# Optimization experiments

Measured on AMD Instinct MI355X. Metric: run time of the kernel, lower is better.

The kernel has to match this reference:

```python
import jax, jax.numpy as jnp
import numpy as np

N_NODES = 100000
N_EDGES = 1250000
NFEAT = 64
NHID = 64


def setup_inputs() -> dict:
    key = jax.random.key(0)
    k1, k2, k3 = jax.random.split(key, 3)
    x = jax.random.normal(k1, (N_NODES, NFEAT), dtype=jnp.float32)
    edge_index = jax.random.randint(k2, (2, N_EDGES), 0, N_NODES, dtype=jnp.int64)
    # Glorot-style init for the GCNConv weight [out, in]
    scale = 1.0 / np.sqrt(NFEAT)
    weight = jax.random.normal(k3, (NHID, NFEAT), dtype=jnp.float32) * scale
    bias = jnp.zeros((NHID,), dtype=jnp.float32)
    return {"x": x, "edge_index": edge_index, "weight": weight, "bias": bias}


def reference(x, edge_index, weight, bias):
    """Single-layer GCNConv: out = D^-1/2 (A+I) D^-1/2 (x W^T) + b."""
    n = x.shape[0]
    # add self-loops
    loop = jnp.arange(n, dtype=edge_index.dtype)
    src = jnp.concatenate([edge_index[0], loop])  # [E+N]
    dst = jnp.concatenate([edge_index[1], loop])
    # linear transform first (cheaper: nfeat -> nhid)
    h = x @ weight.T  # [N, nhid]
    # symmetric normalization with unit edge weights
    ones = jnp.ones_like(dst, dtype=h.dtype)
    deg = jax.ops.segment_sum(ones, dst, num_segments=n)  # [N]
    dinv = jnp.where(deg > 0, jax.lax.rsqrt(jnp.maximum(deg, 1e-12)), 0.0)
    norm = dinv[src] * dinv[dst]  # [E+N]
    # gather -> scale -> scatter-add
    msg = h[src] * norm[:, None]  # [E+N, nhid]
    out = jax.ops.segment_sum(msg, dst, num_segments=n)  # [N, nhid]
    return out + bias
```

## Files before the change

### kernel.cpp

```cpp
#include <hip/hip_runtime.h>

#define NF 64
#define ELLS 48
#define OCAP 65536


__global__ __launch_bounds__(256) void k_ell(const int* __restrict__ src,
                                             const int* __restrict__ dst,
                                             int* degc, int* ocnt, int* oflow,
                                             int* __restrict__ ell, int e, int n) {
    int grp = blockIdx.x & 7;
    int chunk = (n + 7) >> 3;
    int lo = grp * chunk;
    int hi = min(lo + chunk, n);
    int nb = gridDim.x >> 3;
    int bi = blockIdx.x >> 3;
    for (int i = bi * 256 + threadIdx.x; i < e; i += nb * 256) {
        int d = dst[i];
        if (d < lo || d >= hi) continue;
        int s = src[i];
        int slot = atomicAdd(&degc[d], 1);
        if (slot < ELLS) {
            ell[(long)d * ELLS + slot] = s;
        } else {
            int o = atomicAdd(ocnt, 1);
            if (o < OCAP) { oflow[2 * o] = s; oflow[2 * o + 1] = d; }
        }
    }
}

__global__ __launch_bounds__(256) void k_dinv(const int* __restrict__ degc,
                                              float* __restrict__ dinv, int n) {
    int i = blockIdx.x * 256 + threadIdx.x;
    if (i < n) dinv[i] = rsqrtf((float)(degc[i] + 1));
}


__global__ __launch_bounds__(256) void k_agg_gemm(const float* __restrict__ x,
                                                  const float* __restrict__ W,
                                                  const float* __restrict__ bias,
                                                  const float* __restrict__ dinv,
                                                  const int* __restrict__ degc,
                                                  const int* __restrict__ ell,
                                                  float* __restrict__ out, int n) {
    __shared__ float wt[NF * NF];
    __shared__ float vsh[4][NF];
    int tid = threadIdx.x;
    for (int idx = tid; idx < NF * NF; idx += 256) {
        int k = idx >> 6, j = idx & 63;
        wt[idx] = W[j * NF + k];
    }
    int wv = tid >> 6, lane = tid & 63;
    float bj = bias[lane];
    __syncthreads();

    int ngroups = (n + 3) >> 2, gs = gridDim.x;
    int g = blockIdx.x;
    int d = g * 4 + wv;
    int ev = 0, mc = 0;
    if (d < n) {
        if (lane < ELLS) ev = ell[(long)d * ELLS + lane];
        mc = degc[d];
    }
    while (g < ngroups) {
        int gn = g + gs, dn = gn * 4 + wv;
        int evn = 0, mcn = 0;
        if (gn < ngroups && dn < n) {
            if (lane < ELLS) evn = ell[(long)dn * ELLS + lane];
            mcn = degc[dn];
        }
        if (d < n) {
            float dd = rsqrtf((float)(mc + 1));
            int m = min(mc, ELLS);
            float a0 = x[(long)d * NF + lane] * dd;
            float a1 = 0.f, a2 = 0.f, a3 = 0.f, a4 = 0.f, a5 = 0.f, a6 = 0.f, a7 = 0.f;
            for (int j = 0; j < m; j += 8) {
                int s0 = __shfl(ev, j + 0), s1 = __shfl(ev, j + 1);
                int s2 = __shfl(ev, j + 2), s3 = __shfl(ev, j + 3);
                int s4 = __shfl(ev, j + 4), s5 = __shfl(ev, j + 5);
                int s6 = __shfl(ev, j + 6), s7 = __shfl(ev, j + 7);
                bool b0 = j + 0 < m, b1 = j + 1 < m, b2 = j + 2 < m, b3 = j + 3 < m;
                bool b4 = j + 4 < m, b5 = j + 5 < m, b6 = j + 6 < m, b7 = j + 7 < m;
                s0 = b0 ? s0 : 0; s1 = b1 ? s1 : 0; s2 = b2 ? s2 : 0; s3 = b3 ? s3 : 0;
                s4 = b4 ? s4 : 0; s5 = b5 ? s5 : 0; s6 = b6 ? s6 : 0; s7 = b7 ? s7 : 0;
                float w0 = b0 ? dinv[s0] : 0.f, w1 = b1 ? dinv[s1] : 0.f;
                float w2 = b2 ? dinv[s2] : 0.f, w3 = b3 ? dinv[s3] : 0.f;
                float w4 = b4 ? dinv[s4] : 0.f, w5 = b5 ? dinv[s5] : 0.f;
                float w6 = b6 ? dinv[s6] : 0.f, w7 = b7 ? dinv[s7] : 0.f;
                a0 = fmaf(x[(long)s0 * NF + lane], w0, a0);
                a1 = fmaf(x[(long)s1 * NF + lane], w1, a1);
                a2 = fmaf(x[(long)s2 * NF + lane], w2, a2);
                a3 = fmaf(x[(long)s3 * NF + lane], w3, a3);
                a4 = fmaf(x[(long)s4 * NF + lane], w4, a4);
                a5 = fmaf(x[(long)s5 * NF + lane], w5, a5);
                a6 = fmaf(x[(long)s6 * NF + lane], w6, a6);
                a7 = fmaf(x[(long)s7 * NF + lane], w7, a7);
            }
            float v = dd * (((a0 + a1) + (a2 + a3)) + ((a4 + a5) + (a6 + a7)));

            vsh[wv][lane] = v;
            float r = bj;
#pragma unroll
            for (int k0 = 0; k0 < NF; k0 += 4) {
                float4 bv = *reinterpret_cast<const float4*>(&vsh[wv][k0]);
                r = fmaf(bv.x, wt[(k0 + 0) * NF + lane], r);
                r = fmaf(bv.y, wt[(k0 + 1) * NF + lane], r);
                r = fmaf(bv.z, wt[(k0 + 2) * NF + lane], r);
                r = fmaf(bv.w, wt[(k0 + 3) * NF + lane], r);
            }
            out[(long)d * NF + lane] = r;
        }
        g = gn; d = dn; ev = evn; mc = mcn;
    }
}

__global__ __launch_bounds__(64) void k_oflow(const float* __restrict__ x,
                                              const float* __restrict__ W,
                                              const float* __restrict__ dinv,
                                              const int* __restrict__ ocnt,
                                              const int* __restrict__ oflow,
                                              float* out) {
    int c = *ocnt; if (c > OCAP) c = OCAP;
    int lane = threadIdx.x;
    for (int o = blockIdx.x; o < c; o += gridDim.x) {
        int s = oflow[2 * o], d = oflow[2 * o + 1];
        float norm = dinv[s] * dinv[d];
        float r = 0.f;
        for (int k = 0; k < NF; ++k)
            r = fmaf(x[(long)s * NF + k], W[lane * NF + k], r);
        atomicAdd(&out[(long)d * NF + lane], norm * r);
    }
}


extern "C" void kernel_launch(void* const* d_in, const int* in_sizes, int n_in,
                              void* d_out, int out_size, void* d_ws, size_t ws_size,
                              hipStream_t stream) {
    const float* x    = (const float*)d_in[0];
    const int*   ei   = (const int*)d_in[1];
    const float* W    = (const float*)d_in[2];
    const float* bias = (const float*)d_in[3];
    float*       out  = (float*)d_out;

    const int n = in_sizes[0] / NF;
    const int e = in_sizes[1] / 2;
    const int* src = ei;
    const int* dst = ei + e;

    int*   degc  = (int*)d_ws;
    int*   ocnt  = degc + n;
    float* dinv  = (float*)(ocnt + 1);
    int*   oflow = (int*)(dinv + n);
    int*   ell   = oflow + 2 * OCAP;

    dim3 blk(256);
    hipMemsetAsync(degc, 0, (size_t)(n + 1) * sizeof(int), stream);
    k_ell <<<2048, blk, 0, stream>>>(src, dst, degc, ocnt, oflow, ell, e, n);
    k_dinv<<<(n + 255) / 256, blk, 0, stream>>>(degc, dinv, n);
    k_agg_gemm<<<2048, blk, 0, stream>>>(x, W, bias, dinv, degc, ell, out, n);
    k_oflow<<<64, 64, 0, stream>>>(x, W, dinv, ocnt, oflow, out);
}
```

Before: 146.4 us.

## Gather fp16 copy of x, store ELL in output buffer, shuffle dinv

Adds a pre-pass that converts x to fp16 so the neighbour gather in the aggregation kernel reads half as many bytes per row. The ELL adjacency table now lives in the output buffer, widened to 64 slots so each lane holds one neighbour id, instead of a separate 48-slot workspace array. Each lane also loads its neighbour's dinv once, and the value is broadcast with shuffles rather than fetched per edge inside the loop. The trade is an extra conversion pass over x and reduced precision in the gathered features. It also depends on each warp reading its row's ELL entries before overwriting that row.

```diff
diff --git a/kernel.cpp b/kernel.cpp
--- a/kernel.cpp
+++ b/kernel.cpp
@@ -1,14 +1,27 @@
 #include <hip/hip_runtime.h>
+#include <hip/hip_fp16.h>
 
 #define NF 64
-#define ELLS 48
 #define OCAP 65536
+
+__global__ __launch_bounds__(256) void k_half(const float* __restrict__ x,
+                                              __half* __restrict__ xh, int total4) {
+    int i = blockIdx.x * 256 + threadIdx.x;
+    if (i >= total4) return;
+    float4 v = reinterpret_cast<const float4*>(x)[i];
+    __half2 p0 = __floats2half2_rn(v.x, v.y);
+    __half2 p1 = __floats2half2_rn(v.z, v.w);
+    uint2 u;
+    u.x = *reinterpret_cast<unsigned*>(&p0);
+    u.y = *reinterpret_cast<unsigned*>(&p1);
+    reinterpret_cast<uint2*>(xh)[i] = u;
+}
 
 
 __global__ __launch_bounds__(256) void k_ell(const int* __restrict__ src,
                                              const int* __restrict__ dst,
                                              int* degc, int* ocnt, int* oflow,
-                                             int* __restrict__ ell, int e, int n) {
+                                             int* ell, int e, int n) {
     int grp = blockIdx.x & 7;
     int chunk = (n + 7) >> 3;
     int lo = grp * chunk;
@@ -20,8 +33,8 @@
         if (d < lo || d >= hi) continue;
         int s = src[i];
         int slot = atomicAdd(&degc[d], 1);
-        if (slot < ELLS) {
-            ell[(long)d * ELLS + slot] = s;
+        if (slot < NF) {
+            ell[(unsigned)d * NF + slot] = s;
         } else {
             int o = atomicAdd(ocnt, 1);
             if (o < OCAP) { oflow[2 * o] = s; oflow[2 * o + 1] = d; }
@@ -36,13 +49,12 @@
 }
 
 
-__global__ __launch_bounds__(256) void k_agg_gemm(const float* __restrict__ x,
+__global__ __launch_bounds__(256) void k_agg_gemm(const __half* __restrict__ xh,
                                                   const float* __restrict__ W,
                                                   const float* __restrict__ bias,
                                                   const float* __restrict__ dinv,
                                                   const int* __restrict__ degc,
-                                                  const int* __restrict__ ell,
-                                                  float* __restrict__ out, int n) {
+                                                  float* out, int n) {
     __shared__ float wt[NF * NF];
     __shared__ float vsh[4][NF];
     int tid = threadIdx.x;
@@ -50,67 +62,71 @@
         int k = idx >> 6, j = idx & 63;
         wt[idx] = W[j * NF + k];
     }
-    int wv = tid >> 6, lane = tid & 63;
+    int wv_id = tid >> 6;
+    unsigned lane = tid & 63;
     float bj = bias[lane];
     __syncthreads();
 
+    const int* outi = (const int*)out;
     int ngroups = (n + 3) >> 2, gs = gridDim.x;
     int g = blockIdx.x;
-    int d = g * 4 + wv;
-    int ev = 0, mc = 0;
+    int d = g * 4 + wv_id;
+    int ev = 0, mc = 0; float wvv = 0.f;
     if (d < n) {
-        if (lane < ELLS) ev = ell[(long)d * ELLS + lane];
         mc = degc[d];
+        int e0 = outi[(unsigned)d * NF + lane];
+        int m = min(mc, NF);
+        ev = ((int)lane < m) ? e0 : 0;
+        wvv = ((int)lane < m) ? dinv[ev] : 0.f;
     }
     while (g < ngroups) {
-        int gn = g + gs, dn = gn * 4 + wv;
-        int evn = 0, mcn = 0;
+        int gn = g + gs, dn = gn * 4 + wv_id;
+        int evn = 0, mcn = 0; float wvn = 0.f;
         if (gn < ngroups && dn < n) {
-            if (lane < ELLS) evn = ell[(long)dn * ELLS + lane];
             mcn = degc[dn];
+            int e0 = outi[(unsigned)dn * NF + lane];
+            int mn = min(mcn, NF);
+            evn = ((int)lane < mn) ? e0 : 0;
+            wvn = ((int)lane < mn) ? dinv[evn] : 0.f;
         }
         if (d < n) {
             float dd = rsqrtf((float)(mc + 1));
-            int m = min(mc, ELLS);
-            float a0 = x[(long)d * NF + lane] * dd;
+            int m = min(mc, NF);
+            float a0 = __half2float(xh[(unsigned)d * NF + lane]) * dd;
             float a1 = 0.f, a2 = 0.f, a3 = 0.f, a4 = 0.f, a5 = 0.f, a6 = 0.f, a7 = 0.f;
             for (int j = 0; j < m; j += 8) {
                 int s0 = __shfl(ev, j + 0), s1 = __shfl(ev, j + 1);
                 int s2 = __shfl(ev, j + 2), s3 = __shfl(ev, j + 3);
                 int s4 = __shfl(ev, j + 4), s5 = __shfl(ev, j + 5);
                 int s6 = __shfl(ev, j + 6), s7 = __shfl(ev, j + 7);
-                bool b0 = j + 0 < m, b1 = j + 1 < m, b2 = j + 2 < m, b3 = j + 3 < m;
-                bool b4 = j + 4 < m, b5 = j + 5 < m, b6 = j + 6 < m, b7 = j + 7 < m;
-                s0 = b0 ? s0 : 0; s1 = b1 ? s1 : 0; s2 = b2 ? s2 : 0; s3 = b3 ? s3 : 0;
-                s4 = b4 ? s4 : 0; s5 = b5 ? s5 : 0; s6 = b6 ? s6 : 0; s7 = b7 ? s7 : 0;
-                float w0 = b0 ? dinv[s0] : 0.f, w1 = b1 ? dinv[s1] : 0.f;
-                float w2 = b2 ? dinv[s2] : 0.f, w3 = b3 ? dinv[s3] : 0.f;
-                float w4 = b4 ? dinv[s4] : 0.f, w5 = b5 ? dinv[s5] : 0.f;
-                float w6 = b6 ? dinv[s6] : 0.f, w7 = b7 ? dinv[s7] : 0.f;
-                a0 = fmaf(x[(long)s0 * NF + lane], w0, a0);
-                a1 = fmaf(x[(long)s1 * NF + lane], w1, a1);
-                a2 = fmaf(x[(long)s2 * NF + lane], w2, a2);
-                a3 = fmaf(x[(long)s3 * NF + lane], w3, a3);
-                a4 = fmaf(x[(long)s4 * NF + lane], w4, a4);
-                a5 = fmaf(x[(long)s5 * NF + lane], w5, a5);
-                a6 = fmaf(x[(long)s6 * NF + lane], w6, a6);
-                a7 = fmaf(x[(long)s7 * NF + lane], w7, a7);
+                float w0 = __shfl(wvv, j + 0), w1 = __shfl(wvv, j + 1);
+                float w2 = __shfl(wvv, j + 2), w3 = __shfl(wvv, j + 3);
+                float w4 = __shfl(wvv, j + 4), w5 = __shfl(wvv, j + 5);
+                float w6 = __shfl(wvv, j + 6), w7 = __shfl(wvv, j + 7);
+                a0 = fmaf(__half2float(xh[(unsigned)s0 * NF + lane]), w0, a0);
+                a1 = fmaf(__half2float(xh[(unsigned)s1 * NF + lane]), w1, a1);
+                a2 = fmaf(__half2float(xh[(unsigned)s2 * NF + lane]), w2, a2);
+                a3 = fmaf(__half2float(xh[(unsigned)s3 * NF + lane]), w3, a3);
+                a4 = fmaf(__half2float(xh[(unsigned)s4 * NF + lane]), w4, a4);
+                a5 = fmaf(__half2float(xh[(unsigned)s5 * NF + lane]), w5, a5);
+                a6 = fmaf(__half2float(xh[(unsigned)s6 * NF + lane]), w6, a6);
+                a7 = fmaf(__half2float(xh[(unsigned)s7 * NF + lane]), w7, a7);
             }
             float v = dd * (((a0 + a1) + (a2 + a3)) + ((a4 + a5) + (a6 + a7)));
 
-            vsh[wv][lane] = v;
+            vsh[wv_id][lane] = v;
             float r = bj;
 #pragma unroll
             for (int k0 = 0; k0 < NF; k0 += 4) {
-                float4 bv = *reinterpret_cast<const float4*>(&vsh[wv][k0]);
+                float4 bv = *reinterpret_cast<const float4*>(&vsh[wv_id][k0]);
                 r = fmaf(bv.x, wt[(k0 + 0) * NF + lane], r);
                 r = fmaf(bv.y, wt[(k0 + 1) * NF + lane], r);
                 r = fmaf(bv.z, wt[(k0 + 2) * NF + lane], r);
                 r = fmaf(bv.w, wt[(k0 + 3) * NF + lane], r);
             }
-            out[(long)d * NF + lane] = r;
+            out[(unsigned)d * NF + lane] = r;
         }
-        g = gn; d = dn; ev = evn; mc = mcn;
+        g = gn; d = dn; ev = evn; mc = mcn; wvv = wvn;
     }
 }
 
@@ -147,16 +163,18 @@
     const int* src = ei;
     const int* dst = ei + e;
 
-    int*   degc  = (int*)d_ws;
+    __half* xh   = (__half*)d_ws;
+    int*   degc  = (int*)(xh + (size_t)n * NF);
     int*   ocnt  = degc + n;
     float* dinv  = (float*)(ocnt + 1);
     int*   oflow = (int*)(dinv + n);
-    int*   ell   = oflow + 2 * OCAP;
 
     dim3 blk(256);
     hipMemsetAsync(degc, 0, (size_t)(n + 1) * sizeof(int), stream);
-    k_ell <<<2048, blk, 0, stream>>>(src, dst, degc, ocnt, oflow, ell, e, n);
+    int total4 = n * (NF / 4);
+    k_half<<<(total4 + 255) / 256, blk, 0, stream>>>(x, xh, total4);
+    k_ell <<<2048, blk, 0, stream>>>(src, dst, degc, ocnt, oflow, (int*)out, e, n);
     k_dinv<<<(n + 255) / 256, blk, 0, stream>>>(degc, dinv, n);
-    k_agg_gemm<<<2048, blk, 0, stream>>>(x, W, bias, dinv, degc, ell, out, n);
+    k_agg_gemm<<<2048, blk, 0, stream>>>(xh, W, bias, dinv, degc, out, n);
     k_oflow<<<64, 64, 0, stream>>>(x, W, dinv, ocnt, oflow, out);
 }
```

Measured after the change: 170.3 us. 1.16x slower.

## Store ELL lists in the output buffer and split aggregation from the GEMM

Applied to the files above, without the earlier changes.

The ELL neighbour lists are now written directly into the output buffer, widened to 64 slots per node. The aggregation kernel reads each node's list from its own output row and overwrites that row in place with the aggregated features. A separate GEMM kernel then applies W and the bias to four rows per wave. This frees the separate ELL workspace, sends fewer edges to overflow, and gives the aggregation kernel more occupancy because it no longer uses shared memory. The cost is an extra launch plus a full read and write of the output for the GEMM pass.

```diff
diff --git a/kernel.cpp b/kernel.cpp
--- a/kernel.cpp
+++ b/kernel.cpp
@@ -1,14 +1,12 @@
 #include <hip/hip_runtime.h>
 
 #define NF 64
-#define ELLS 48
 #define OCAP 65536
-
 
 __global__ __launch_bounds__(256) void k_ell(const int* __restrict__ src,
                                              const int* __restrict__ dst,
                                              int* degc, int* ocnt, int* oflow,
-                                             int* __restrict__ ell, int e, int n) {
+                                             int* ell, int e, int n) {
     int grp = blockIdx.x & 7;
     int chunk = (n + 7) >> 3;
     int lo = grp * chunk;
@@ -20,8 +18,8 @@
         if (d < lo || d >= hi) continue;
         int s = src[i];
         int slot = atomicAdd(&degc[d], 1);
-        if (slot < ELLS) {
-            ell[(long)d * ELLS + slot] = s;
+        if (slot < NF) {
+            ell[(unsigned)d * NF + slot] = s;
         } else {
             int o = atomicAdd(ocnt, 1);
             if (o < OCAP) { oflow[2 * o] = s; oflow[2 * o + 1] = d; }
@@ -36,43 +34,32 @@
 }
 
 
-__global__ __launch_bounds__(256) void k_agg_gemm(const float* __restrict__ x,
-                                                  const float* __restrict__ W,
-                                                  const float* __restrict__ bias,
-                                                  const float* __restrict__ dinv,
-                                                  const int* __restrict__ degc,
-                                                  const int* __restrict__ ell,
-                                                  float* __restrict__ out, int n) {
-    __shared__ float wt[NF * NF];
-    __shared__ float vsh[4][NF];
-    int tid = threadIdx.x;
-    for (int idx = tid; idx < NF * NF; idx += 256) {
-        int k = idx >> 6, j = idx & 63;
-        wt[idx] = W[j * NF + k];
-    }
-    int wv = tid >> 6, lane = tid & 63;
-    float bj = bias[lane];
-    __syncthreads();
-
+__global__ __launch_bounds__(256) void k_agg(const float* __restrict__ x,
+                                             const float* __restrict__ dinv,
+                                             const int* __restrict__ degc,
+                                             float* out, int n) {
+    int wv = threadIdx.x >> 6;
+    unsigned lane = threadIdx.x & 63;
+    const int* outi = (const int*)out;
     int ngroups = (n + 3) >> 2, gs = gridDim.x;
     int g = blockIdx.x;
     int d = g * 4 + wv;
     int ev = 0, mc = 0;
     if (d < n) {
-        if (lane < ELLS) ev = ell[(long)d * ELLS + lane];
+        ev = outi[(unsigned)d * NF + lane];
         mc = degc[d];
     }
     while (g < ngroups) {
         int gn = g + gs, dn = gn * 4 + wv;
         int evn = 0, mcn = 0;
         if (gn < ngroups && dn < n) {
-            if (lane < ELLS) evn = ell[(long)dn * ELLS + lane];
+            evn = outi[(unsigned)dn * NF + lane];
             mcn = degc[dn];
         }
         if (d < n) {
             float dd = rsqrtf((float)(mc + 1));
-            int m = min(mc, ELLS);
-            float a0 = x[(long)d * NF + lane] * dd;
+            int m = min(mc, NF);
+            float a0 = x[(unsigned)d * NF + lane] * dd;
             float a1 = 0.f, a2 = 0.f, a3 = 0.f, a4 = 0.f, a5 = 0.f, a6 = 0.f, a7 = 0.f;
             for (int j = 0; j < m; j += 8) {
                 int s0 = __shfl(ev, j + 0), s1 = __shfl(ev, j + 1);
@@ -87,30 +74,69 @@
                 float w2 = b2 ? dinv[s2] : 0.f, w3 = b3 ? dinv[s3] : 0.f;
                 float w4 = b4 ? dinv[s4] : 0.f, w5 = b5 ? dinv[s5] : 0.f;
                 float w6 = b6 ? dinv[s6] : 0.f, w7 = b7 ? dinv[s7] : 0.f;
-                a0 = fmaf(x[(long)s0 * NF + lane], w0, a0);
-                a1 = fmaf(x[(long)s1 * NF + lane], w1, a1);
-                a2 = fmaf(x[(long)s2 * NF + lane], w2, a2);
-                a3 = fmaf(x[(long)s3 * NF + lane], w3, a3);
-                a4 = fmaf(x[(long)s4 * NF + lane], w4, a4);
-                a5 = fmaf(x[(long)s5 * NF + lane], w5, a5);
-                a6 = fmaf(x[(long)s6 * NF + lane], w6, a6);
-                a7 = fmaf(x[(long)s7 * NF + lane], w7, a7);
+                a0 = fmaf(x[(unsigned)s0 * NF + lane], w0, a0);
+                a1 = fmaf(x[(unsigned)s1 * NF + lane], w1, a1);
+                a2 = fmaf(x[(unsigned)s2 * NF + lane], w2, a2);
+                a3 = fmaf(x[(unsigned)s3 * NF + lane], w3, a3);
+                a4 = fmaf(x[(unsigned)s4 * NF + lane], w4, a4);
+                a5 = fmaf(x[(unsigned)s5 * NF + lane], w5, a5);
+                a6 = fmaf(x[(unsigned)s6 * NF + lane], w6, a6);
+                a7 = fmaf(x[(unsigned)s7 * NF + lane], w7, a7);
             }
             float v = dd * (((a0 + a1) + (a2 + a3)) + ((a4 + a5) + (a6 + a7)));
-
-            vsh[wv][lane] = v;
-            float r = bj;
-#pragma unroll
-            for (int k0 = 0; k0 < NF; k0 += 4) {
-                float4 bv = *reinterpret_cast<const float4*>(&vsh[wv][k0]);
-                r = fmaf(bv.x, wt[(k0 + 0) * NF + lane], r);
-                r = fmaf(bv.y, wt[(k0 + 1) * NF + lane], r);
-                r = fmaf(bv.z, wt[(k0 + 2) * NF + lane], r);
-                r = fmaf(bv.w, wt[(k0 + 3) * NF + lane], r);
-            }
-            out[(long)d * NF + lane] = r;
+            out[(unsigned)d * NF + lane] = v;
         }
         g = gn; d = dn; ev = evn; mc = mcn;
+    }
+}
+
+
+__global__ __launch_bounds__(256) void k_gemm(const float* __restrict__ W,
+                                              const float* __restrict__ bias,
+                                              float* out, int n) {
+    __shared__ float wt[NF * NF];
+    __shared__ float vsh[4][4][NF];
+    int tid = threadIdx.x;
+    for (int idx = tid; idx < NF * NF; idx += 256) {
+        int k = idx >> 6, j = idx & 63;
+        wt[idx] = W[j * NF + k];
+    }
+    int wv = tid >> 6;
+    unsigned lane = tid & 63;
+    float bj = bias[lane];
+    __syncthreads();
+
+    int ntiles = (n + 15) >> 4, gs = gridDim.x;
+    for (int t = blockIdx.x; t < ntiles; t += gs) {
+        int r = t * 16 + wv * 4;
+        float v0 = (r + 0 < n) ? out[(unsigned)(r + 0) * NF + lane] : 0.f;
+        float v1 = (r + 1 < n) ? out[(unsigned)(r + 1) * NF + lane] : 0.f;
+        float v2 = (r + 2 < n) ? out[(unsigned)(r + 2) * NF + lane] : 0.f;
+        float v3 = (r + 3 < n) ? out[(unsigned)(r + 3) * NF + lane] : 0.f;
+        vsh[wv][0][lane] = v0;
+        vsh[wv][1][lane] = v1;
+        vsh[wv][2][lane] = v2;
+        vsh[wv][3][lane] = v3;
+        float r0 = bj, r1 = bj, r2 = bj, r3 = bj;
+#pragma unroll
+        for (int k0 = 0; k0 < NF; k0 += 4) {
+            float4 b0 = *reinterpret_cast<const float4*>(&vsh[wv][0][k0]);
+            float4 b1 = *reinterpret_cast<const float4*>(&vsh[wv][1][k0]);
+            float4 b2 = *reinterpret_cast<const float4*>(&vsh[wv][2][k0]);
+            float4 b3 = *reinterpret_cast<const float4*>(&vsh[wv][3][k0]);
+            float q0 = wt[(k0 + 0) * NF + lane];
+            float q1 = wt[(k0 + 1) * NF + lane];
+            float q2 = wt[(k0 + 2) * NF + lane];
+            float q3 = wt[(k0 + 3) * NF + lane];
+            r0 = fmaf(b0.x, q0, r0); r0 = fmaf(b0.y, q1, r0); r0 = fmaf(b0.z, q2, r0); r0 = fmaf(b0.w, q3, r0);
+            r1 = fmaf(b1.x, q0, r1); r1 = fmaf(b1.y, q1, r1); r1 = fmaf(b1.z, q2, r1); r1 = fmaf(b1.w, q3, r1);
+            r2 = fmaf(b2.x, q0, r2); r2 = fmaf(b2.y, q1, r2); r2 = fmaf(b2.z, q2, r2); r2 = fmaf(b2.w, q3, r2);
+            r3 = fmaf(b3.x, q0, r3); r3 = fmaf(b3.y, q1, r3); r3 = fmaf(b3.z, q2, r3); r3 = fmaf(b3.w, q3, r3);
+        }
+        if (r + 0 < n) out[(unsigned)(r + 0) * NF + lane] = r0;
+        if (r + 1 < n) out[(unsigned)(r + 1) * NF + lane] = r1;
+        if (r + 2 < n) out[(unsigned)(r + 2) * NF + lane] = r2;
+        if (r + 3 < n) out[(unsigned)(r + 3) * NF + lane] = r3;
     }
 }
 
@@ -151,12 +177,12 @@
     int*   ocnt  = degc + n;
     float* dinv  = (float*)(ocnt + 1);
     int*   oflow = (int*)(dinv + n);
-    int*   ell   = oflow + 2 * OCAP;
 
     dim3 blk(256);
     hipMemsetAsync(degc, 0, (size_t)(n + 1) * sizeof(int), stream);
-    k_ell <<<2048, blk, 0, stream>>>(src, dst, degc, ocnt, oflow, ell, e, n);
+    k_ell <<<2048, blk, 0, stream>>>(src, dst, degc, ocnt, oflow, (int*)out, e, n);
     k_dinv<<<(n + 255) / 256, blk, 0, stream>>>(degc, dinv, n);
-    k_agg_gemm<<<2048, blk, 0, stream>>>(x, W, bias, dinv, degc, ell, out, n);
+    k_agg <<<2048, blk, 0, stream>>>(x, dinv, degc, out, n);
+    k_gemm<<<(n + 15) / 16, blk, 0, stream>>>(W, bias, out, n);
     k_oflow<<<64, 64, 0, stream>>>(x, W, dinv, ocnt, oflow, out);
 }
```

New measurement: 228.3 us. 1.56x slower.

## Prescale features by inverse degree and store ELL lists in output buffer

Applied to the files above, without the earlier changes.

A new pass writes x scaled by each row's inverse square-root degree into a workspace copy, with an extra zero padding row. The aggregation loop can then sum prescaled rows directly, with no per-neighbour dinv gather and no predicated weights; out-of-range neighbour slots point at the zero row. The ELL neighbour table now lives in the output buffer, widened to 64 slots per row to match the row width. Overflow capacity is sized from the remaining workspace. The cost is an extra full read and write of x in the scaling pass, plus reliance on reading each row's indices before that row is overwritten.

```diff
diff --git a/kernel.cpp b/kernel.cpp
--- a/kernel.cpp
+++ b/kernel.cpp
@@ -1,14 +1,13 @@
 #include <hip/hip_runtime.h>
+#include <stdint.h>
 
 #define NF 64
-#define ELLS 48
-#define OCAP 65536
 
 
 __global__ __launch_bounds__(256) void k_ell(const int* __restrict__ src,
                                              const int* __restrict__ dst,
-                                             int* degc, int* ocnt, int* oflow,
-                                             int* __restrict__ ell, int e, int n) {
+                                             int* degc, int* ocnt, int* oflow, int ocap,
+                                             int* ell, int e, int n) {
     int grp = blockIdx.x & 7;
     int chunk = (n + 7) >> 3;
     int lo = grp * chunk;
@@ -20,29 +19,37 @@
         if (d < lo || d >= hi) continue;
         int s = src[i];
         int slot = atomicAdd(&degc[d], 1);
-        if (slot < ELLS) {
-            ell[(long)d * ELLS + slot] = s;
+        if (slot < NF) {
+            ell[(unsigned)d * NF + slot] = s;
         } else {
             int o = atomicAdd(ocnt, 1);
-            if (o < OCAP) { oflow[2 * o] = s; oflow[2 * o + 1] = d; }
+            if (o < ocap) { oflow[2 * o] = s; oflow[2 * o + 1] = d; }
         }
     }
 }
 
-__global__ __launch_bounds__(256) void k_dinv(const int* __restrict__ degc,
-                                              float* __restrict__ dinv, int n) {
+__global__ __launch_bounds__(256) void k_scale(const float* __restrict__ x,
+                                               const int* __restrict__ degc,
+                                               float* __restrict__ xs, int n) {
     int i = blockIdx.x * 256 + threadIdx.x;
-    if (i < n) dinv[i] = rsqrtf((float)(degc[i] + 1));
+    int total = (n + 1) * (NF / 4);
+    if (i >= total) return;
+    int row = i >> 4;
+    float4 v = {0.f, 0.f, 0.f, 0.f};
+    if (row < n) {
+        float dd = rsqrtf((float)(degc[row] + 1));
+        v = reinterpret_cast<const float4*>(x)[i];
+        v.x *= dd; v.y *= dd; v.z *= dd; v.w *= dd;
+    }
+    reinterpret_cast<float4*>(xs)[i] = v;
 }
 
 
-__global__ __launch_bounds__(256) void k_agg_gemm(const float* __restrict__ x,
+__global__ __launch_bounds__(256) void k_agg_gemm(const float* __restrict__ xs,
                                                   const float* __restrict__ W,
                                                   const float* __restrict__ bias,
-                                                  const float* __restrict__ dinv,
                                                   const int* __restrict__ degc,
-                                                  const int* __restrict__ ell,
-                                                  float* __restrict__ out, int n) {
+                                                  float* out, int n) {
     __shared__ float wt[NF * NF];
     __shared__ float vsh[4][NF];
     int tid = threadIdx.x;
@@ -50,51 +57,53 @@
         int k = idx >> 6, j = idx & 63;
         wt[idx] = W[j * NF + k];
     }
-    int wv = tid >> 6, lane = tid & 63;
+    int wv = tid >> 6;
+    unsigned lane = tid & 63;
     float bj = bias[lane];
     __syncthreads();
 
+    const int* outi = (const int*)out;
     int ngroups = (n + 3) >> 2, gs = gridDim.x;
     int g = blockIdx.x;
     int d = g * 4 + wv;
     int ev = 0, mc = 0;
     if (d < n) {
-        if (lane < ELLS) ev = ell[(long)d * ELLS + lane];
+        ev = outi[(unsigned)d * NF + lane];
         mc = degc[d];
     }
     while (g < ngroups) {
         int gn = g + gs, dn = gn * 4 + wv;
         int evn = 0, mcn = 0;
         if (gn < ngroups && dn < n) {
-            if (lane < ELLS) evn = ell[(long)dn * ELLS + lane];
+            evn = outi[(unsigned)dn * NF + lane];
             mcn = degc[dn];
         }
         if (d < n) {
             float dd = rsqrtf((float)(mc + 1));
-            int m = min(mc, ELLS);
-            float a0 = x[(long)d * NF + lane] * dd;
+            int m = min(mc, NF);
+            float a0 = xs[(unsigned)d * NF + lane];
             float a1 = 0.f, a2 = 0.f, a3 = 0.f, a4 = 0.f, a5 = 0.f, a6 = 0.f, a7 = 0.f;
             for (int j = 0; j < m; j += 8) {
                 int s0 = __shfl(ev, j + 0), s1 = __shfl(ev, j + 1);
                 int s2 = __shfl(ev, j + 2), s3 = __shfl(ev, j + 3);
                 int s4 = __shfl(ev, j + 4), s5 = __shfl(ev, j + 5);
                 int s6 = __shfl(ev, j + 6), s7 = __shfl(ev, j + 7);
-                bool b0 = j + 0 < m, b1 = j + 1 < m, b2 = j + 2 < m, b3 = j + 3 < m;
-                bool b4 = j + 4 < m, b5 = j + 5 < m, b6 = j + 6 < m, b7 = j + 7 < m;
-                s0 = b0 ? s0 : 0; s1 = b1 ? s1 : 0; s2 = b2 ? s2 : 0; s3 = b3 ? s3 : 0;
-                s4 = b4 ? s4 : 0; s5 = b5 ? s5 : 0; s6 = b6 ? s6 : 0; s7 = b7 ? s7 : 0;
-                float w0 = b0 ? dinv[s0] : 0.f, w1 = b1 ? dinv[s1] : 0.f;
-                float w2 = b2 ? dinv[s2] : 0.f, w3 = b3 ? dinv[s3] : 0.f;
-                float w4 = b4 ? dinv[s4] : 0.f, w5 = b5 ? dinv[s5] : 0.f;
-                float w6 = b6 ? dinv[s6] : 0.f, w7 = b7 ? dinv[s7] : 0.f;
-                a0 = fmaf(x[(long)s0 * NF + lane], w0, a0);
-                a1 = fmaf(x[(long)s1 * NF + lane], w1, a1);
-                a2 = fmaf(x[(long)s2 * NF + lane], w2, a2);
-                a3 = fmaf(x[(long)s3 * NF + lane], w3, a3);
-                a4 = fmaf(x[(long)s4 * NF + lane], w4, a4);
-                a5 = fmaf(x[(long)s5 * NF + lane], w5, a5);
-                a6 = fmaf(x[(long)s6 * NF + lane], w6, a6);
-                a7 = fmaf(x[(long)s7 * NF + lane], w7, a7);
+                s0 = (j + 0 < m) ? s0 : n;
+                s1 = (j + 1 < m) ? s1 : n;
+                s2 = (j + 2 < m) ? s2 : n;
+                s3 = (j + 3 < m) ? s3 : n;
+                s4 = (j + 4 < m) ? s4 : n;
+                s5 = (j + 5 < m) ? s5 : n;
+                s6 = (j + 6 < m) ? s6 : n;
+                s7 = (j + 7 < m) ? s7 : n;
+                a0 += xs[(unsigned)s0 * NF + lane];
+                a1 += xs[(unsigned)s1 * NF + lane];
+                a2 += xs[(unsigned)s2 * NF + lane];
+                a3 += xs[(unsigned)s3 * NF + lane];
+                a4 += xs[(unsigned)s4 * NF + lane];
+                a5 += xs[(unsigned)s5 * NF + lane];
+                a6 += xs[(unsigned)s6 * NF + lane];
+                a7 += xs[(unsigned)s7 * NF + lane];
             }
             float v = dd * (((a0 + a1) + (a2 + a3)) + ((a4 + a5) + (a6 + a7)));
 
@@ -108,7 +117,7 @@
                 r = fmaf(bv.z, wt[(k0 + 2) * NF + lane], r);
                 r = fmaf(bv.w, wt[(k0 + 3) * NF + lane], r);
             }
-            out[(long)d * NF + lane] = r;
+            out[(unsigned)d * NF + lane] = r;
         }
         g = gn; d = dn; ev = evn; mc = mcn;
     }
@@ -116,15 +125,15 @@
 
 __global__ __launch_bounds__(64) void k_oflow(const float* __restrict__ x,
                                               const float* __restrict__ W,
-                                              const float* __restrict__ dinv,
+                                              const int* __restrict__ degc,
                                               const int* __restrict__ ocnt,
-                                              const int* __restrict__ oflow,
+                                              const int* __restrict__ oflow, int ocap,
                                               float* out) {
-    int c = *ocnt; if (c > OCAP) c = OCAP;
+    int c = *ocnt; if (c > ocap) c = ocap;
     int lane = threadIdx.x;
     for (int o = blockIdx.x; o < c; o += gridDim.x) {
         int s = oflow[2 * o], d = oflow[2 * o + 1];
-        float norm = dinv[s] * dinv[d];
+        float norm = rsqrtf((float)(degc[s] + 1)) * rsqrtf((float)(degc[d] + 1));
         float r = 0.f;
         for (int k = 0; k < NF; ++k)
             r = fmaf(x[(long)s * NF + k], W[lane * NF + k], r);
@@ -147,16 +156,19 @@
     const int* src = ei;
     const int* dst = ei + e;
 
-    int*   degc  = (int*)d_ws;
-    int*   ocnt  = degc + n;
-    float* dinv  = (float*)(ocnt + 1);
-    int*   oflow = (int*)(dinv + n);
-    int*   ell   = oflow + 2 * OCAP;
+    int*   degc = (int*)d_ws;
+    int*   ocnt = degc + n;
+    uintptr_t p = ((uintptr_t)(ocnt + 1) + 255) & ~(uintptr_t)255;
+    float* xs   = (float*)p;
+    int*   oflow = (int*)(xs + (size_t)(n + 1) * NF);
+    long   rest = (long)ws_size - ((char*)oflow - (char*)d_ws);
+    int    ocap = rest > 0 ? (int)(rest / 8) : 0;
 
     dim3 blk(256);
     hipMemsetAsync(degc, 0, (size_t)(n + 1) * sizeof(int), stream);
-    k_ell <<<2048, blk, 0, stream>>>(src, dst, degc, ocnt, oflow, ell, e, n);
-    k_dinv<<<(n + 255) / 256, blk, 0, stream>>>(degc, dinv, n);
-    k_agg_gemm<<<2048, blk, 0, stream>>>(x, W, bias, dinv, degc, ell, out, n);
-    k_oflow<<<64, 64, 0, stream>>>(x, W, dinv, ocnt, oflow, out);
+    k_ell  <<<2048, blk, 0, stream>>>(src, dst, degc, ocnt, oflow, ocap, (int*)out, e, n);
+    int total4 = (n + 1) * (NF / 4);
+    k_scale<<<(total4 + 255) / 256, blk, 0, stream>>>(x, degc, xs, n);
+    k_agg_gemm<<<2048, blk, 0, stream>>>(xs, W, bias, degc, out, n);
+    k_oflow<<<64, 64, 0, stream>>>(x, W, degc, ocnt, oflow, ocap, out);
 }
```

Result: slower. 150.4 us (+2.7%).
